# Kernel tuning notes

Measured on AMD Instinct MI355X. Metric: run time of the kernel, lower is better.

Reference implementation:

```python
import jax, jax.numpy as jnp
import numpy as np

QMAX = 127.0

def _sym_quantize(t):
    # per-tensor symmetric int8 fake-quant: returns (quantized values as float, scale)
    scale = jnp.max(jnp.abs(t)) / QMAX
    q = jnp.clip(jnp.round(t / scale), -QMAX, QMAX)
    return q, scale

def setup_inputs() -> dict:
    key = jax.random.key(0)
    k1, k2, k3 = jax.random.split(key, 3)
    TOKENS, IN_F, OUT_F = 4096, 4096, 4096
    x = jax.random.normal(k1, (TOKENS, IN_F), dtype=jnp.float32)
    # int8-valued weight buffer (stored int32 for portability), symmetric range
    quantized_weight = jax.random.randint(k2, (OUT_F, IN_F), -127, 128, dtype=jnp.int32)
    weight_scale = jnp.float32(0.01)  # scalar per-tensor weight scale buffer
    bias = jax.random.normal(k3, (OUT_F,), dtype=jnp.float32)
    return {"x": x, "quantized_weight": quantized_weight,
            "weight_scale": weight_scale, "bias": bias}

def reference(x, quantized_weight, weight_scale, bias):
    q_x, x_scale = _sym_quantize(x)                      # [T, In] fake-quant activations
    w = quantized_weight.astype(jnp.float32)             # [Out, In]
    out = jnp.matmul(q_x, w.T)                           # fp32 GEMM on int8-valued operands
    out = out * (x_scale * weight_scale)                 # dequant scaling
    out = out + bias
    return out
```

## Files before the change

kernel.cpp:

```cpp
#include <hip/hip_runtime.h>

typedef __attribute__((ext_vector_type(4))) int int4v;

#define NB_MAX 1024

__device__ __forceinline__ void async_ld16(const void* g, void* l) {
  __builtin_amdgcn_global_load_lds(
      (const __attribute__((address_space(1))) void*)g,
      (__attribute__((address_space(3))) void*)l,
      16, 0, 0);
}

__global__ void absmax_partial_kernel(const float* __restrict__ x,
                                      float* __restrict__ partial, int n4) {
  const float4* x4 = (const float4*)x;
  float m = 0.0f;
  for (int i = blockIdx.x * blockDim.x + threadIdx.x; i < n4;
       i += gridDim.x * blockDim.x) {
    float4 v = x4[i];
    m = fmaxf(m, fabsf(v.x));
    m = fmaxf(m, fabsf(v.y));
    m = fmaxf(m, fabsf(v.z));
    m = fmaxf(m, fabsf(v.w));
  }
#pragma unroll
  for (int off = 32; off > 0; off >>= 1)
    m = fmaxf(m, __shfl_down(m, off, 64));
  __shared__ float wmax[4];
  const int wid = threadIdx.x >> 6;
  if ((threadIdx.x & 63) == 0) wmax[wid] = m;
  __syncthreads();
  if (threadIdx.x == 0)
    partial[blockIdx.x] =
        fmaxf(fmaxf(wmax[0], wmax[1]), fmaxf(wmax[2], wmax[3]));
}

__device__ __forceinline__ float reduce_partials(const float* partial) {
  __shared__ float smax;
  float m = 0.0f;
  for (int i = threadIdx.x; i < NB_MAX; i += blockDim.x)
    m = fmaxf(m, partial[i]);
#pragma unroll
  for (int off = 32; off > 0; off >>= 1)
    m = fmaxf(m, __shfl_down(m, off, 64));
  __shared__ float wmax[4];
  const int wid = threadIdx.x >> 6;
  if ((threadIdx.x & 63) == 0) wmax[wid] = m;
  __syncthreads();
  if (threadIdx.x == 0)
    smax = fmaxf(fmaxf(wmax[0], wmax[1]), fmaxf(wmax[2], wmax[3]));
  __syncthreads();
  return smax;
}

__global__ void quant_pack_kernel(const float* __restrict__ x,
                                  const int* __restrict__ w,
                                  const float* __restrict__ partial,
                                  float* __restrict__ scale_slot,
                                  int* __restrict__ qx, int* __restrict__ qw,
                                  int nx4, int nw4) {
  const float scale = reduce_partials(partial) / 127.0f;
  const int i = blockIdx.x * blockDim.x + threadIdx.x;
  if (i == 0) *scale_slot = scale;
  if (i < nx4) {
    float4 v = ((const float4*)x)[i];
    int q0 = (int)fminf(fmaxf(rintf(v.x / scale), -127.0f), 127.0f);
    int q1 = (int)fminf(fmaxf(rintf(v.y / scale), -127.0f), 127.0f);
    int q2 = (int)fminf(fmaxf(rintf(v.z / scale), -127.0f), 127.0f);
    int q3 = (int)fminf(fmaxf(rintf(v.w / scale), -127.0f), 127.0f);
    unsigned int p = (unsigned int)(q0 & 255) |
                     ((unsigned int)(q1 & 255) << 8) |
                     ((unsigned int)(q2 & 255) << 16) |
                     ((unsigned int)(q3 & 255) << 24);
    qx[i] = (int)p;
  }
  if (i < nw4) {
    int4 v = ((const int4*)w)[i];
    unsigned int p = (unsigned int)(v.x & 255) |
                     ((unsigned int)(v.y & 255) << 8) |
                     ((unsigned int)(v.z & 255) << 16) |
                     ((unsigned int)(v.w & 255) << 24);
    qw[i] = (int)p;
  }
}

__global__ __launch_bounds__(256) void gemm_i8_kernel(
    const signed char* __restrict__ A,
    const signed char* __restrict__ B,
    const float* __restrict__ bias,
    const float* __restrict__ scale_slot,
    const float* __restrict__ wscale,
    float* __restrict__ out, int K, int N) {
  __shared__ signed char As[128 * 128];
  __shared__ signed char Bs[128 * 128];

  const int tid = threadIdx.x;
  const int lane = tid & 63;
  const int wid = tid >> 6;
  const int row0 = blockIdx.y * 128;
  const int col0 = blockIdx.x * 128;
  const int wm = (wid >> 1) * 64;
  const int wn = (wid & 1) * 64;

  int4v acc[4][4] = {};

  const int gchunk = ((lane & 7) ^ ((lane >> 3) & 7)) * 16;
  const signed char* gA =
      A + (long)(row0 + wid * 32 + (lane >> 3)) * K + gchunk;
  const signed char* gB =
      B + (long)(col0 + wid * 32 + (lane >> 3)) * K + gchunk;
  const int ldsw = wid * 4096;

  const int q = lane >> 4;
  const int c7 = lane & 7;
  const int frow = (wm + (lane & 15)) * 128;
  const int fcs0 = ((q ^ c7) << 4);
  const int fcs1 = (((4 + q) ^ c7) << 4);
  const int fbrow = (wn + (lane & 15)) * 128;

  for (int k0 = 0; k0 < K; k0 += 128) {
    __syncthreads();
#pragma unroll
    for (int t = 0; t < 4; t++) {
      async_ld16(gA + k0 + t * 8 * (long)K, As + ldsw + t * 1024);
      async_ld16(gB + k0 + t * 8 * (long)K, Bs + ldsw + t * 1024);
    }
    asm volatile("s_waitcnt vmcnt(0)" ::: "memory");
    __syncthreads();

#pragma unroll
    for (int s = 0; s < 2; s++) {
      const int ca = (s == 0) ? fcs0 : fcs1;
      int4v a[4], b[4];
#pragma unroll
      for (int i = 0; i < 4; i++) {
        a[i] = *(const int4v*)(As + frow + i * 16 * 128 + ca);
        b[i] = *(const int4v*)(Bs + fbrow + i * 16 * 128 + ca);
      }
#pragma unroll
      for (int i = 0; i < 4; i++)
#pragma unroll
        for (int j = 0; j < 4; j++)
          acc[i][j] = __builtin_amdgcn_mfma_i32_16x16x64_i8(a[i], b[j],
                                                            acc[i][j], 0, 0, 0);
    }
  }

  const float s = scale_slot[0] * wscale[0];
  const int orow = row0 + wm + ((lane >> 4) << 2);
  const int ocol0 = col0 + wn + (lane & 15);
#pragma unroll
  for (int j = 0; j < 4; j++) {
    const int c = ocol0 + j * 16;
    const float bv = bias[c];
#pragma unroll
    for (int i = 0; i < 4; i++) {
#pragma unroll
      for (int r = 0; r < 4; r++) {
        out[(long)(orow + i * 16 + r) * N + c] = (float)acc[i][j][r] * s + bv;
      }
    }
  }
}

extern "C" void kernel_launch(void* const* d_in, const int* in_sizes, int n_in,
                              void* d_out, int out_size, void* d_ws,
                              size_t ws_size, hipStream_t stream) {
  const float* x = (const float*)d_in[0];
  const int* w = (const int*)d_in[1];
  const float* wscale = (const float*)d_in[2];
  const float* bias = (const float*)d_in[3];
  float* out = (float*)d_out;

  const int OUT_F = in_sizes[3];
  const int IN_F = in_sizes[1] / OUT_F;
  const int TOKENS = in_sizes[0] / IN_F;

  float* partial = (float*)d_ws;
  float* scale_slot = partial + NB_MAX;
  signed char* qx = (signed char*)d_ws + 8192;
  signed char* qw = qx + (size_t)TOKENS * IN_F;

  const int nx4 = TOKENS * IN_F / 4;
  const int nw4 = OUT_F * IN_F / 4;

  absmax_partial_kernel<<<NB_MAX, 256, 0, stream>>>(x, partial, nx4);

  const int nmax = nx4 > nw4 ? nx4 : nw4;
  quant_pack_kernel<<<(nmax + 255) / 256, 256, 0, stream>>>(
      x, w, partial, scale_slot, (int*)qx, (int*)qw, nx4, nw4);

  dim3 grid(OUT_F / 128, TOKENS / 128);
  gemm_i8_kernel<<<grid, 256, 0, stream>>>(qx, qw, bias, scale_slot, wscale,
                                           out, IN_F, OUT_F);
}
```

Baseline: 259.2 us.

## Register-prefetch next K tile to overlap global loads with MFMA compute

Replaces the direct global-to-LDS async loads with a software pipeline. Each iteration now issues global loads for the next K tile into registers, computes MFMAs on the current LDS tile, then stores the prefetched registers to LDS. This is meant to hide global memory latency behind compute instead of waiting on vmcnt(0) each iteration. It costs extra VGPRs for staging and VALU/LDS store instructions, and it keeps a single LDS buffer with two barriers per iteration.

Result: no change. 264.3 us (+2.0%).

```diff
diff --git a/kernel.cpp b/kernel.cpp
--- a/kernel.cpp
+++ b/kernel.cpp
@@ -3,13 +3,6 @@
 typedef __attribute__((ext_vector_type(4))) int int4v;
 
 #define NB_MAX 1024
-
-__device__ __forceinline__ void async_ld16(const void* g, void* l) {
-  __builtin_amdgcn_global_load_lds(
-      (const __attribute__((address_space(1))) void*)g,
-      (__attribute__((address_space(3))) void*)l,
-      16, 0, 0);
-}
 
 __global__ void absmax_partial_kernel(const float* __restrict__ x,
                                       float* __restrict__ partial, int n4) {
@@ -110,41 +103,64 @@
   const signed char* gB =
       B + (long)(col0 + wid * 32 + (lane >> 3)) * K + gchunk;
   const int ldsw = wid * 4096;
+  const long rstride = 8 * (long)K;
 
   const int q = lane >> 4;
   const int c7 = lane & 7;
   const int frow = (wm + (lane & 15)) * 128;
+  const int fbrow = (wn + (lane & 15)) * 128;
   const int fcs0 = ((q ^ c7) << 4);
   const int fcs1 = (((4 + q) ^ c7) << 4);
-  const int fbrow = (wn + (lane & 15)) * 128;
-
-  for (int k0 = 0; k0 < K; k0 += 128) {
+
+  int4v rA[4], rB[4];
+
+#define LOAD_TILE(k0)                                      \
+  {                                                        \
+    _Pragma("unroll") for (int t = 0; t < 4; t++) {        \
+      rA[t] = *(const int4v*)(gA + (k0) + t * rstride);    \
+      rB[t] = *(const int4v*)(gB + (k0) + t * rstride);    \
+    }                                                      \
+  }
+
+#define STORE_LDS()                                              \
+  {                                                              \
+    _Pragma("unroll") for (int t = 0; t < 4; t++) {              \
+      *(int4v*)(As + ldsw + t * 1024 + lane * 16) = rA[t];       \
+      *(int4v*)(Bs + ldsw + t * 1024 + lane * 16) = rB[t];       \
+    }                                                            \
+  }
+
+#define COMPUTE()                                                          \
+  {                                                                        \
+    _Pragma("unroll") for (int s = 0; s < 2; s++) {                        \
+      const int ca = (s == 0) ? fcs0 : fcs1;                               \
+      int4v a[4], b[4];                                                    \
+      _Pragma("unroll") for (int i = 0; i < 4; i++) {                      \
+        a[i] = *(const int4v*)(As + frow + i * 16 * 128 + ca);             \
+        b[i] = *(const int4v*)(Bs + fbrow + i * 16 * 128 + ca);            \
+      }                                                                    \
+      _Pragma("unroll") for (int i = 0; i < 4; i++)                        \
+          _Pragma("unroll") for (int j = 0; j < 4; j++) acc[i][j] =        \
+          __builtin_amdgcn_mfma_i32_16x16x64_i8(a[i], b[j], acc[i][j], 0,  \
+                                                0, 0);                     \
+    }                                                                      \
+  }
+
+  LOAD_TILE(0)
+  STORE_LDS()
+  __syncthreads();
+
+  for (int k0 = 128; k0 < K; k0 += 128) {
+    LOAD_TILE(k0)
+    COMPUTE()
     __syncthreads();
-#pragma unroll
-    for (int t = 0; t < 4; t++) {
-      async_ld16(gA + k0 + t * 8 * (long)K, As + ldsw + t * 1024);
-      async_ld16(gB + k0 + t * 8 * (long)K, Bs + ldsw + t * 1024);
-    }
-    asm volatile("s_waitcnt vmcnt(0)" ::: "memory");
+    STORE_LDS()
     __syncthreads();
-
-#pragma unroll
-    for (int s = 0; s < 2; s++) {
-      const int ca = (s == 0) ? fcs0 : fcs1;
-      int4v a[4], b[4];
-#pragma unroll
-      for (int i = 0; i < 4; i++) {
-        a[i] = *(const int4v*)(As + frow + i * 16 * 128 + ca);
-        b[i] = *(const int4v*)(Bs + fbrow + i * 16 * 128 + ca);
-      }
-#pragma unroll
-      for (int i = 0; i < 4; i++)
-#pragma unroll
-        for (int j = 0; j < 4; j++)
-          acc[i][j] = __builtin_amdgcn_mfma_i32_16x16x64_i8(a[i], b[j],
-                                                            acc[i][j], 0, 0, 0);
-    }
-  }
+  }
+  COMPUTE()
+#undef LOAD_TILE
+#undef STORE_LDS
+#undef COMPUTE
 
   const float s = scale_slot[0] * wscale[0];
   const int orow = row0 + wm + ((lane >> 4) << 2);
```
